# Kernel optimization log

Hardware: AMD Instinct MI355X
Metric: run time of the kernel (lower is better)

## Reference

```python
import jax, jax.numpy as jnp
import numpy as np

B, L, D, K, V = 256, 50, 128, 4, 50000
LENGTH = 5      # opt.length
BETA = 0.01     # opt.beta scaling on loss1
EPS = 1e-12     # F.normalize eps


def _l2norm(x, axis):
    n = jnp.sqrt(jnp.sum(x * x, axis=axis, keepdims=True))
    return x / jnp.maximum(n, EPS)


def setup_inputs() -> dict:
    key = jax.random.key(0)
    ks = jax.random.split(key, 11)
    s = 1.0 / np.sqrt(D)  # reset_parameters: uniform(-stdv, stdv)
    u = lambda k, shape: jax.random.uniform(k, shape, jnp.float32, -s, s)
    return {
        "hidden": jax.random.normal(ks[0], (B, L, D), jnp.float32),
        "mask": jnp.ones((B, L), jnp.int32),
        "pos_emb": u(ks[1], (L, D)),
        "w1": u(ks[2], (2 * D, D)),
        "w2": u(ks[3], (D, K)),
        "glu1_w": u(ks[4], (D, K * D)),
        "glu1_b": u(ks[5], (K * D,)),
        "att_w1": u(ks[6], (D, D)),
        "att_w2": u(ks[7], (D, D)),
        "att_v": u(ks[8], (D, K)),
        "emb": u(ks[9], (V, D)),
    }


def reference(hidden, mask, pos_emb, w1, w2, glu1_w, glu1_b, att_w1, att_w2, att_v, emb):
    m = mask.astype(jnp.float32)[..., None]                       # [B,L,1]
    hs = jnp.sum(hidden * m, axis=1) / jnp.sum(m, axis=1)         # [B,D] masked mean
    # nh = tanh(cat(pos, hidden) @ w1); then sigmoid(glu1)
    cat = jnp.concatenate([jnp.broadcast_to(pos_emb[None], hidden.shape), hidden], axis=-1)
    nh = jnp.tanh(cat @ w1)                                       # [B,L,D]
    nh = jax.nn.sigmoid(nh @ glu1_w + glu1_b)                     # [B,L,K*D]
    # torch.split(dim=2) + stack(dim=3) -> [B,L,D,K]
    nh = nh.reshape(B, L, K, D).transpose(0, 1, 3, 2)             # [B,L,D,K]
    beta = jnp.einsum('bldk,dk->blk', nh, w2)                     # [B,L,K]
    # attention gate alpha = sigmoid(att_v(tanh(W1 hs + W2 hidden)))
    att = jnp.tanh(hs[:, None, :] @ att_w1 + hidden @ att_w2)     # [B,L,D]
    alpha = jax.nn.sigmoid(att @ att_v)                           # [B,L,K]
    beta = beta * (0.5 + alpha) * m                               # mask over interests
    # per-interest L2 normalize along sequence (fused over K)
    nb = _l2norm(beta, axis=1)                                    # [B,L,K]
    # pairwise |cos| between interests: vectorized Gram instead of python loops
    G = jnp.einsum('bli,blj->bij', nb, nb)                        # [B,K,K]
    triu = jnp.triu(jnp.ones((K, K), jnp.float32), 1)
    sim = jnp.sum(jnp.abs(G) * triu, axis=(1, 2)) * (2.0 / (K * (K - 1)))  # [B]
    lens = jnp.sum(mask, axis=1).astype(jnp.float32) - LENGTH     # sumask[:,0] - length
    loss1 = jnp.sum(jax.nn.sigmoid(sim * lens))                   # scalar
    # per-interest pooled session reps, stacked on leading axis -> [K,B,D]
    select = jnp.einsum('blk,bld->kbd', beta, hidden)
    b_norm = _l2norm(emb[1:], axis=-1)                            # [V-1,D]
    scores = jnp.einsum('kbd,vd->kbv', select, b_norm)            # [K,B,V-1]
    max_scores = jnp.max(scores, axis=0)                          # [B,V-1]
    return (max_scores, loss1 * BETA, scores)
```

## Files before the change

kernel.cpp:

```cpp
#include <hip/hip_runtime.h>
#include <hip/hip_bf16.h>
#include <math.h>

constexpr int NB = 256;
constexpr int NL = 50;
constexpr int ND = 128;
constexpr int NK = 4;
constexpr int NVm1 = 49999;
constexpr int NPAD2 = 50176;
constexpr int ROWS = NB * NL;
constexpr int MROWS = NB * NK;
constexpr int GEMM_NT = 4;
constexpr int MR = 64;

constexpr int G_BN  = NPAD2 / 2;
constexpr int G_HS  = NB / 2;
constexpr int G_PP  = NL / 2;
constexpr int G_XB  = ROWS * ND / 2048;
constexpr int G_W1T = ND * ND / 256;
constexpr int G_AWT = ND * ND / 256;
constexpr int G_GLT = ND * 512 / 256;
constexpr int G_TOT = G_BN + G_HS + G_PP + G_XB + G_W1T + G_AWT + G_GLT;

typedef __bf16 bf16x8 __attribute__((ext_vector_type(8)));
typedef float f32x4 __attribute__((ext_vector_type(4)));

__device__ __forceinline__ float sigm_fast(float x) { return 1.0f / (1.0f + __expf(-x)); }
__device__ __forceinline__ float sigm_prec(float x) { return 1.0f / (1.0f + expf(-x)); }
__device__ __forceinline__ float fast_tanh(float x) {
    float xc = fminf(fmaxf(x, -15.f), 15.f);
    float e = __expf(2.f * xc);
    return (e - 1.f) / (e + 1.f);
}

__device__ __forceinline__ void gld_lds16(const void* g, void* l) {
    __builtin_amdgcn_global_load_lds(
        (const __attribute__((address_space(1))) void*)g,
        (__attribute__((address_space(3))) void*)l, 16, 0, 0);
}

__global__ __launch_bounds__(256) void k_prep(
    const float* __restrict__ hidden, const int* __restrict__ mask,
    const float* __restrict__ pos_emb, const float* __restrict__ w1,
    const float* __restrict__ att_w2, const float* __restrict__ glu1_w,
    const float* __restrict__ emb,
    float* __restrict__ hs, float* __restrict__ posPart,
    __hip_bfloat16* __restrict__ XbG, __hip_bfloat16* __restrict__ w1h_t,
    __hip_bfloat16* __restrict__ attw2_t, __hip_bfloat16* __restrict__ glu_t,
    __hip_bfloat16* __restrict__ bnv, float* __restrict__ loss_out) {
    __shared__ float sPP[2 * ND];
    __shared__ float red[4];
    int blk = blockIdx.x, tid = threadIdx.x;
    if (blk < G_BN) {
        int v = blk * 2 + (tid >> 7);
        int j = tid & 127;
        float x = 0.f;
        if (v < NVm1) x = emb[((size_t)v + 1) * ND + j];
        float ss = x * x;
        for (int off = 32; off >= 1; off >>= 1) ss += __shfl_xor(ss, off);
        if ((tid & 63) == 0) red[tid >> 6] = ss;
        __syncthreads();
        float tot = (tid < 128) ? (red[0] + red[1]) : (red[2] + red[3]);
        float rn = 1.f / fmaxf(sqrtf(tot), 1e-12f);
        bnv[(size_t)v * ND + j] = __float2bfloat16(x * rn);
    } else if (blk < G_BN + G_HS) {
        int b = (blk - G_BN) * 2 + (tid >> 7);
        int d = tid & 127;
        float acc = 0.f, msum = 0.f;
        for (int l = 0; l < NL; ++l) {
            float mv = (float)mask[b * NL + l];
            acc += hidden[((size_t)b * NL + l) * ND + d] * mv;
            msum += mv;
        }
        hs[b * ND + d] = acc / msum;
        if (blk == G_BN && tid == 0) loss_out[0] = 0.f;
    } else if (blk < G_BN + G_HS + G_PP) {
        int rel = blk - (G_BN + G_HS);
        int rl = tid >> 7, d = tid & 127;
        int r = rel * 2 + rl;
        sPP[rl * ND + d] = pos_emb[r * ND + d];
        __syncthreads();
        float acc = 0.f;
#pragma unroll 8
        for (int j = 0; j < ND; ++j) acc += sPP[rl * ND + j] * w1[j * ND + d];
        posPart[r * ND + d] = acc;
    } else if (blk < G_BN + G_HS + G_PP + G_XB) {
        int rel = blk - (G_BN + G_HS + G_PP);
        size_t base = (size_t)rel * 2048 + (size_t)tid * 8;
        float4 f0 = *(const float4*)&hidden[base];
        float4 f1 = *(const float4*)&hidden[base + 4];
        union { bf16x8 v; __hip_bfloat16 h[8]; } u;
        u.h[0] = __float2bfloat16(f0.x); u.h[1] = __float2bfloat16(f0.y);
        u.h[2] = __float2bfloat16(f0.z); u.h[3] = __float2bfloat16(f0.w);
        u.h[4] = __float2bfloat16(f1.x); u.h[5] = __float2bfloat16(f1.y);
        u.h[6] = __float2bfloat16(f1.z); u.h[7] = __float2bfloat16(f1.w);
        *(bf16x8*)&XbG[base] = u.v;
    } else if (blk < G_BN + G_HS + G_PP + G_XB + G_W1T) {
        int i = (blk - (G_BN + G_HS + G_PP + G_XB)) * 256 + tid;
        int d = i >> 7, j = i & 127;
        w1h_t[d * ND + j] = __float2bfloat16(w1[(ND + j) * ND + d]);
    } else if (blk < G_BN + G_HS + G_PP + G_XB + G_W1T + G_AWT) {
        int i = (blk - (G_BN + G_HS + G_PP + G_XB + G_W1T)) * 256 + tid;
        int d = i >> 7, j = i & 127;
        attw2_t[d * ND + j] = __float2bfloat16(att_w2[j * ND + d]);
    } else {
        int i = (blk - (G_BN + G_HS + G_PP + G_XB + G_W1T + G_AWT)) * 256 + tid;
        int c = i >> 7, j = i & 127;
        glu_t[c * ND + j] = __float2bfloat16(glu1_w[j * 512 + c]);
    }
}

__global__ __launch_bounds__(256) void k_mega(
    const __hip_bfloat16* __restrict__ XbG, const __hip_bfloat16* __restrict__ w1h_t,
    const __hip_bfloat16* __restrict__ attw2_t, const __hip_bfloat16* __restrict__ glu_t,
    const float* __restrict__ hs, const float* __restrict__ att_w1,
    const float* __restrict__ att_v, const float* __restrict__ posPart,
    const float* __restrict__ glu1_b, const float* __restrict__ w2,
    const int* __restrict__ mask, float* __restrict__ beta_out) {
    __shared__ __hip_bfloat16 XbS[MR * ND];
    __shared__ __hip_bfloat16 WS[ND * ND];
    __shared__ __attribute__((aligned(16))) __hip_bfloat16 NHS[MR * 136];
    __shared__ float alphaS[MR * NK];
    __shared__ float hsW1S[3 * ND];
    int row0 = blockIdx.x * MR;
    int tid = threadIdx.x;
    int wave = tid >> 6, lane = tid & 63, l16 = lane & 15, quad = lane >> 4;
    int b0 = row0 / NL;

#pragma unroll
    for (int it = 0; it < 4; ++it) {
        int id = it * 256 + tid;
        int row = id >> 4, c = id & 15, gc = c ^ (row & 7);
        gld_lds16((const char*)XbG + ((size_t)(row0 + row) * 16 + gc) * 16,
                  (char*)XbS + (size_t)(it * 256 + wave * 64) * 16);
    }
#pragma unroll
    for (int it = 0; it < 8; ++it) {
        int id = it * 256 + tid;
        int row = id >> 4, c = id & 15, gc = c ^ (row & 7);
        gld_lds16((const char*)attw2_t + ((size_t)row * 16 + gc) * 16,
                  (char*)WS + (size_t)(it * 256 + wave * 64) * 16);
    }
    for (int i = tid; i < 3 * ND; i += 256) {
        int bb = i >> 7, d = i & 127, b = b0 + bb;
        float acc = 0.f;
        if (b < NB) {
            for (int j = 0; j < ND; ++j) acc += hs[b * ND + j] * att_w1[j * ND + d];
        }
        hsW1S[i] = acc;
    }
    __syncthreads();

    const bf16x8* Xv = (const bf16x8*)XbS;
    const bf16x8* Wv = (const bf16x8*)WS;
    const bf16x8* Nv = (const bf16x8*)NHS;
    int arow = wave * 16 + l16;

    f32x4 acc8[8];
#pragma unroll
    for (int ni = 0; ni < 8; ++ni) acc8[ni] = (f32x4){0.f, 0.f, 0.f, 0.f};
#pragma unroll
    for (int kk = 0; kk < 4; ++kk) {
        int ko = kk * 4 + quad;
        bf16x8 af = Xv[arow * 16 + (ko ^ (arow & 7))];
#pragma unroll
        for (int ni = 0; ni < 8; ++ni) {
            int n = ni * 16 + l16;
            bf16x8 bf = Wv[n * 16 + (ko ^ (n & 7))];
            acc8[ni] = __builtin_amdgcn_mfma_f32_16x16x32_bf16(af, bf, acc8[ni], 0, 0, 0);
        }
    }
#pragma unroll
    for (int r = 0; r < 4; ++r) {
        int lrow = wave * 16 + quad * 4 + r;
        int grow = row0 + lrow;
        int bb = grow / NL - b0;
        float a0 = 0.f, a1 = 0.f, a2 = 0.f, a3 = 0.f;
#pragma unroll
        for (int ni = 0; ni < 8; ++ni) {
            int col = ni * 16 + l16;
            float atv = fast_tanh(hsW1S[bb * ND + col] + acc8[ni][r]);
            float4 av = *(const float4*)&att_v[col * 4];
            a0 += atv * av.x; a1 += atv * av.y; a2 += atv * av.z; a3 += atv * av.w;
        }
#pragma unroll
        for (int off = 1; off < 16; off <<= 1) {
            a0 += __shfl_xor(a0, off); a1 += __shfl_xor(a1, off);
            a2 += __shfl_xor(a2, off); a3 += __shfl_xor(a3, off);
        }
        if (l16 == 0) {
            alphaS[lrow * 4 + 0] = sigm_fast(a0);
            alphaS[lrow * 4 + 1] = sigm_fast(a1);
            alphaS[lrow * 4 + 2] = sigm_fast(a2);
            alphaS[lrow * 4 + 3] = sigm_fast(a3);
        }
    }
    __syncthreads();
#pragma unroll
    for (int it = 0; it < 8; ++it) {
        int id = it * 256 + tid;
        int row = id >> 4, c = id & 15, gc = c ^ (row & 7);
        gld_lds16((const char*)w1h_t + ((size_t)row * 16 + gc) * 16,
                  (char*)WS + (size_t)(it * 256 + wave * 64) * 16);
    }
    __syncthreads();
#pragma unroll
    for (int ni = 0; ni < 8; ++ni) acc8[ni] = (f32x4){0.f, 0.f, 0.f, 0.f};
#pragma unroll
    for (int kk = 0; kk < 4; ++kk) {
        int ko = kk * 4 + quad;
        bf16x8 af = Xv[arow * 16 + (ko ^ (arow & 7))];
#pragma unroll
        for (int ni = 0; ni < 8; ++ni) {
            int n = ni * 16 + l16;
            bf16x8 bf = Wv[n * 16 + (ko ^ (n & 7))];
            acc8[ni] = __builtin_amdgcn_mfma_f32_16x16x32_bf16(af, bf, acc8[ni], 0, 0, 0);
        }
    }
#pragma unroll
    for (int r = 0; r < 4; ++r) {
        int lrow = wave * 16 + quad * 4 + r;
        int grow = row0 + lrow;
        int l = grow % NL;
#pragma unroll
        for (int ni = 0; ni < 8; ++ni) {
            int col = ni * 16 + l16;
            float nhv = fast_tanh(posPart[l * ND + col] + acc8[ni][r]);
            NHS[lrow * 136 + col] = __float2bfloat16(nhv);
        }
    }
    __syncthreads();
    for (int ch = 0; ch < 4; ++ch) {
#pragma unroll
        for (int it = 0; it < 8; ++it) {
            int id = it * 256 + tid;
            int row = id >> 4, c = id & 15, gc = c ^ (row & 7);
            gld_lds16((const char*)glu_t + ((size_t)(ch * ND + row) * 16 + gc) * 16,
                      (char*)WS + (size_t)(it * 256 + wave * 64) * 16);
        }
        __syncthreads();
#pragma unroll
        for (int ni = 0; ni < 8; ++ni) acc8[ni] = (f32x4){0.f, 0.f, 0.f, 0.f};
#pragma unroll
        for (int kk = 0; kk < 4; ++kk) {
            int ko = kk * 4 + quad;
            bf16x8 af = Nv[arow * 17 + ko];
#pragma unroll
            for (int ni = 0; ni < 8; ++ni) {
                int n = ni * 16 + l16;
                bf16x8 bf = Wv[n * 16 + (ko ^ (n & 7))];
                acc8[ni] = __builtin_amdgcn_mfma_f32_16x16x32_bf16(af, bf, acc8[ni], 0, 0, 0);
            }
        }
#pragma unroll
        for (int r = 0; r < 4; ++r) {
            float s = 0.f;
#pragma unroll
            for (int ni = 0; ni < 8; ++ni) {
                int col = ni * 16 + l16;
                s += sigm_fast(acc8[ni][r] + glu1_b[ch * ND + col]) * w2[col * 4 + ch];
            }
#pragma unroll
            for (int off = 1; off < 16; off <<= 1) s += __shfl_xor(s, off);
            if (l16 == 0) {
                int lrow = wave * 16 + quad * 4 + r;
                int grow = row0 + lrow;
                float a = alphaS[lrow * 4 + ch];
                beta_out[(size_t)grow * 4 + ch] = s * (0.5f + a) * (float)mask[grow];
            }
        }
        __syncthreads();
    }
}

__global__ void k_loss(const float* __restrict__ beta, const int* __restrict__ mask,
                       float* __restrict__ loss_out) {
    int b = blockIdx.x;
    int t = threadIdx.x;
    float mv = (t < NL) ? (float)mask[b * NL + t] : 0.f;
    float msum = mv;
    for (int off = 32; off >= 1; off >>= 1) msum += __shfl_xor(msum, off);
    float lens = msum - 5.0f;
    float bk[NK] = {0.f, 0.f, 0.f, 0.f};
    if (t < NL) {
#pragma unroll
        for (int k = 0; k < NK; ++k) bk[k] = beta[((size_t)b * NL + t) * NK + k];
    }
    float nb[NK];
#pragma unroll
    for (int k = 0; k < NK; ++k) {
        float v = bk[k] * bk[k];
        for (int off = 32; off >= 1; off >>= 1) v += __shfl_xor(v, off);
        nb[k] = bk[k] / fmaxf(sqrtf(v), 1e-12f);
    }
    float sim = 0.f;
#pragma unroll
    for (int i = 0; i < NK; ++i) {
#pragma unroll
        for (int j = 0; j < NK; ++j) {
            if (j > i) {
                float p = nb[i] * nb[j];
                for (int off = 32; off >= 1; off >>= 1) p += __shfl_xor(p, off);
                sim += fabsf(p);
            }
        }
    }
    sim *= (2.0f / (NK * (NK - 1)));
    if (t == 0) atomicAdd(loss_out, sigm_prec(sim * lens) * 0.01f);
}

__global__ __launch_bounds__(256) void k_select(
    const float* __restrict__ beta, const float* __restrict__ hidden,
    __hip_bfloat16* __restrict__ selb) {
    int b = blockIdx.x * 2 + (threadIdx.x >> 7);
    int d = threadIdx.x & 127;
    float a0 = 0.f, a1 = 0.f, a2 = 0.f, a3 = 0.f;
    for (int l = 0; l < NL; ++l) {
        float h = hidden[((size_t)b * NL + l) * ND + d];
        const float* bp = &beta[((size_t)b * NL + l) * NK];
        a0 = fmaf(bp[0], h, a0);
        a1 = fmaf(bp[1], h, a1);
        a2 = fmaf(bp[2], h, a2);
        a3 = fmaf(bp[3], h, a3);
    }
    selb[((size_t)b * NK + 0) * ND + d] = __float2bfloat16(a0);
    selb[((size_t)b * NK + 1) * ND + d] = __float2bfloat16(a1);
    selb[((size_t)b * NK + 2) * ND + d] = __float2bfloat16(a2);
    selb[((size_t)b * NK + 3) * ND + d] = __float2bfloat16(a3);
}

__global__ __launch_bounds__(256) void k_gemm(
    const __hip_bfloat16* __restrict__ selb, const __hip_bfloat16* __restrict__ bn,
    float* __restrict__ scores, float* __restrict__ maxs) {
    __shared__ __hip_bfloat16 As[128 * 128];
    __shared__ __hip_bfloat16 Bs[128 * 128];
    int bm0 = blockIdx.y * 128;
    int nbase = blockIdx.x * (128 * GEMM_NT);
    int tid = threadIdx.x;
    int wave = tid >> 6, lane = tid & 63;
    int l16 = lane & 15, quad = lane >> 4;
    int m_loc = (wave >> 1) * 64;
    int n_loc = (wave & 1) * 64;

#pragma unroll
    for (int it = 0; it < 8; ++it) {
        int id = it * 256 + tid;
        int row = id >> 4, c = id & 15, gc = c ^ (row & 7);
        gld_lds16((const char*)selb + ((size_t)(bm0 + row) * 16 + gc) * 16,
                  (char*)As + (size_t)(it * 256 + wave * 64) * 16);
    }

    const bf16x8* Av = (const bf16x8*)As;
    const bf16x8* Bv = (const bf16x8*)Bs;

    for (int nt = 0; nt < GEMM_NT; ++nt) {
        int bn0 = nbase + nt * 128;
#pragma unroll
        for (int it = 0; it < 8; ++it) {
            int id = it * 256 + tid;
            int row = id >> 4, c = id & 15, gc = c ^ (row & 7);
            gld_lds16((const char*)bn + ((size_t)(bn0 + row) * 16 + gc) * 16,
                      (char*)Bs + (size_t)(it * 256 + wave * 64) * 16);
        }
        __syncthreads();

        f32x4 acc[4][4];
#pragma unroll
        for (int mi = 0; mi < 4; ++mi)
#pragma unroll
            for (int ni = 0; ni < 4; ++ni) acc[mi][ni] = (f32x4){0.f, 0.f, 0.f, 0.f};

#pragma unroll
        for (int kk = 0; kk < 4; ++kk) {
            int ko = kk * 4 + quad;
            bf16x8 afr[4], bfr[4];
#pragma unroll
            for (int mi = 0; mi < 4; ++mi) {
                int row = m_loc + mi * 16 + l16;
                afr[mi] = Av[row * 16 + (ko ^ (row & 7))];
            }
#pragma unroll
            for (int ni = 0; ni < 4; ++ni) {
                int row = n_loc + ni * 16 + l16;
                bfr[ni] = Bv[row * 16 + (ko ^ (row & 7))];
            }
#pragma unroll
            for (int mi = 0; mi < 4; ++mi)
#pragma unroll
                for (int ni = 0; ni < 4; ++ni)
                    acc[mi][ni] = __builtin_amdgcn_mfma_f32_16x16x32_bf16(
                        afr[mi], bfr[ni], acc[mi][ni], 0, 0, 0);
        }

#pragma unroll
        for (int mi = 0; mi < 4; ++mi) {
            int m_base = bm0 + m_loc + mi * 16;
            int bidx = (m_base >> 2) + quad;
#pragma unroll
            for (int ni = 0; ni < 4; ++ni) {
                int n = bn0 + n_loc + ni * 16 + l16;
                if (n < NVm1) {
                    float mx = acc[mi][ni][0];
#pragma unroll
                    for (int r = 0; r < 4; ++r) {
                        float val = acc[mi][ni][r];
                        scores[(size_t)r * NB * NVm1 + (size_t)bidx * NVm1 + n] = val;
                        mx = fmaxf(mx, val);
                    }
                    maxs[(size_t)bidx * NVm1 + n] = mx;
                }
            }
        }
        __syncthreads();
    }
}

extern "C" void kernel_launch(void* const* d_in, const int* in_sizes, int n_in,
                              void* d_out, int out_size, void* d_ws, size_t ws_size,
                              hipStream_t stream) {
    const float* hidden  = (const float*)d_in[0];
    const int*   mask    = (const int*)d_in[1];
    const float* pos_emb = (const float*)d_in[2];
    const float* w1      = (const float*)d_in[3];
    const float* w2      = (const float*)d_in[4];
    const float* glu1_w  = (const float*)d_in[5];
    const float* glu1_b  = (const float*)d_in[6];
    const float* att_w1  = (const float*)d_in[7];
    const float* att_w2  = (const float*)d_in[8];
    const float* att_v   = (const float*)d_in[9];
    const float* emb     = (const float*)d_in[10];

    float* out      = (float*)d_out;
    float* max_out  = out;
    float* loss_out = out + (size_t)NB * NVm1;
    float* scores   = out + (size_t)NB * NVm1 + 1;

    char* w = (char*)d_ws;
    auto alloc = [&](size_t bytes) {
        char* p = w;
        w += (bytes + 255) & ~(size_t)255;
        return p;
    };
    float* posPart = (float*)alloc((size_t)NL * ND * 4);
    float* hs      = (float*)alloc((size_t)NB * ND * 4);
    float* betav   = (float*)alloc((size_t)ROWS * NK * 4);
    __hip_bfloat16* XbG     = (__hip_bfloat16*)alloc((size_t)ROWS * ND * 2);
    __hip_bfloat16* w1h_t   = (__hip_bfloat16*)alloc((size_t)ND * ND * 2);
    __hip_bfloat16* attw2_t = (__hip_bfloat16*)alloc((size_t)ND * ND * 2);
    __hip_bfloat16* glu_t   = (__hip_bfloat16*)alloc((size_t)512 * ND * 2);
    __hip_bfloat16* selb    = (__hip_bfloat16*)alloc((size_t)MROWS * ND * 2);
    __hip_bfloat16* bnv     = (__hip_bfloat16*)alloc((size_t)NPAD2 * ND * 2);

    k_prep<<<G_TOT, 256, 0, stream>>>(hidden, mask, pos_emb, w1, att_w2, glu1_w, emb,
                                      hs, posPart, XbG, w1h_t, attw2_t, glu_t, bnv, loss_out);
    k_mega<<<ROWS / MR, 256, 0, stream>>>(XbG, w1h_t, attw2_t, glu_t, hs, att_w1,
                                          att_v, posPart, glu1_b, w2, mask, betav);
    k_loss<<<NB, 64, 0, stream>>>(betav, mask, loss_out);
    k_select<<<NB / 2, 256, 0, stream>>>(betav, hidden, selb);
    k_gemm<<<dim3(NPAD2 / (128 * GEMM_NT), MROWS / 128), 256, 0, stream>>>(selb, bnv, scores, max_out);
}
```

Baseline: 435.8 us.

## Double-buffer GEMM B tiles with nontemporal stores and vectorize embedding normalization

The scores GEMM now streams B in 64-column chunks through a double-buffered LDS tile. The next chunk's global-to-LDS load is issued before the current chunk's MFMAs, and full tiles wait with a partial vmcnt so the score stores stay in flight. Score and max outputs use nontemporal stores to cut cache pollution on the large output write. The embedding normalization in k_prep moves from a 2-rows-per-block LDS reduction to 8 rows per block using float4 loads and a 32-lane shuffle, and k_select reads beta as float4. The hand-tuned vmcnt value depends on the exact count of outstanding stores and loads, so any miscount could race.

```diff
diff --git a/kernel.cpp b/kernel.cpp
--- a/kernel.cpp
+++ b/kernel.cpp
@@ -10,10 +10,10 @@
 constexpr int NPAD2 = 50176;
 constexpr int ROWS = NB * NL;
 constexpr int MROWS = NB * NK;
-constexpr int GEMM_NT = 4;
+constexpr int GEMM_NSPAN = 512;
 constexpr int MR = 64;
 
-constexpr int G_BN  = NPAD2 / 2;
+constexpr int G_BN  = NPAD2 / 8;
 constexpr int G_HS  = NB / 2;
 constexpr int G_PP  = NL / 2;
 constexpr int G_XB  = ROWS * ND / 2048;
@@ -49,20 +49,22 @@
     __hip_bfloat16* __restrict__ attw2_t, __hip_bfloat16* __restrict__ glu_t,
     __hip_bfloat16* __restrict__ bnv, float* __restrict__ loss_out) {
     __shared__ float sPP[2 * ND];
-    __shared__ float red[4];
     int blk = blockIdx.x, tid = threadIdx.x;
     if (blk < G_BN) {
-        int v = blk * 2 + (tid >> 7);
-        int j = tid & 127;
-        float x = 0.f;
-        if (v < NVm1) x = emb[((size_t)v + 1) * ND + j];
-        float ss = x * x;
-        for (int off = 32; off >= 1; off >>= 1) ss += __shfl_xor(ss, off);
-        if ((tid & 63) == 0) red[tid >> 6] = ss;
-        __syncthreads();
-        float tot = (tid < 128) ? (red[0] + red[1]) : (red[2] + red[3]);
-        float rn = 1.f / fmaxf(sqrtf(tot), 1e-12f);
-        bnv[(size_t)v * ND + j] = __float2bfloat16(x * rn);
+        int v = blk * 8 + (tid >> 5);
+        int j = (tid & 31) << 2;
+        float4 x = make_float4(0.f, 0.f, 0.f, 0.f);
+        if (v < NVm1) x = *(const float4*)&emb[((size_t)v + 1) * ND + j];
+        float ss = x.x * x.x + x.y * x.y + x.z * x.z + x.w * x.w;
+#pragma unroll
+        for (int off = 16; off >= 1; off >>= 1) ss += __shfl_xor(ss, off);
+        float rn = 1.f / fmaxf(sqrtf(ss), 1e-12f);
+        union { ushort4 u4; __hip_bfloat16 h[4]; } o;
+        o.h[0] = __float2bfloat16(x.x * rn);
+        o.h[1] = __float2bfloat16(x.y * rn);
+        o.h[2] = __float2bfloat16(x.z * rn);
+        o.h[3] = __float2bfloat16(x.w * rn);
+        *(ushort4*)&bnv[(size_t)v * ND + j] = o.u4;
     } else if (blk < G_BN + G_HS) {
         int b = (blk - G_BN) * 2 + (tid >> 7);
         int d = tid & 127;
@@ -317,11 +319,11 @@
     float a0 = 0.f, a1 = 0.f, a2 = 0.f, a3 = 0.f;
     for (int l = 0; l < NL; ++l) {
         float h = hidden[((size_t)b * NL + l) * ND + d];
-        const float* bp = &beta[((size_t)b * NL + l) * NK];
-        a0 = fmaf(bp[0], h, a0);
-        a1 = fmaf(bp[1], h, a1);
-        a2 = fmaf(bp[2], h, a2);
-        a3 = fmaf(bp[3], h, a3);
+        float4 bv = *(const float4*)&beta[((size_t)b * NL + l) * NK];
+        a0 = fmaf(bv.x, h, a0);
+        a1 = fmaf(bv.y, h, a1);
+        a2 = fmaf(bv.z, h, a2);
+        a3 = fmaf(bv.w, h, a3);
     }
     selb[((size_t)b * NK + 0) * ND + d] = __float2bfloat16(a0);
     selb[((size_t)b * NK + 1) * ND + d] = __float2bfloat16(a1);
@@ -332,15 +334,16 @@
 __global__ __launch_bounds__(256) void k_gemm(
     const __hip_bfloat16* __restrict__ selb, const __hip_bfloat16* __restrict__ bn,
     float* __restrict__ scores, float* __restrict__ maxs) {
-    __shared__ __hip_bfloat16 As[128 * 128];
-    __shared__ __hip_bfloat16 Bs[128 * 128];
+    __shared__ __attribute__((aligned(16))) __hip_bfloat16 As[128 * 128];
+    __shared__ __attribute__((aligned(16))) __hip_bfloat16 Bs[2][64 * 128];
     int bm0 = blockIdx.y * 128;
-    int nbase = blockIdx.x * (128 * GEMM_NT);
+    int nbase = blockIdx.x * GEMM_NSPAN;
     int tid = threadIdx.x;
     int wave = tid >> 6, lane = tid & 63;
     int l16 = lane & 15, quad = lane >> 4;
-    int m_loc = (wave >> 1) * 64;
-    int n_loc = (wave & 1) * 64;
+    int m_loc = wave * 32;
+    bool full = (nbase + GEMM_NSPAN) <= NVm1;
+    const size_t SC_K = (size_t)NB * NVm1;
 
 #pragma unroll
     for (int it = 0; it < 8; ++it) {
@@ -349,69 +352,89 @@
         gld_lds16((const char*)selb + ((size_t)(bm0 + row) * 16 + gc) * 16,
                   (char*)As + (size_t)(it * 256 + wave * 64) * 16);
     }
+#pragma unroll
+    for (int it = 0; it < 4; ++it) {
+        int id = it * 256 + tid;
+        int row = id >> 4, c = id & 15, gc = c ^ (row & 7);
+        gld_lds16((const char*)bn + ((size_t)(nbase + row) * 16 + gc) * 16,
+                  (char*)Bs[0] + (size_t)(it * 256 + wave * 64) * 16);
+    }
+    __syncthreads();
 
     const bf16x8* Av = (const bf16x8*)As;
-    const bf16x8* Bv = (const bf16x8*)Bs;
-
-    for (int nt = 0; nt < GEMM_NT; ++nt) {
-        int bn0 = nbase + nt * 128;
-#pragma unroll
-        for (int it = 0; it < 8; ++it) {
-            int id = it * 256 + tid;
-            int row = id >> 4, c = id & 15, gc = c ^ (row & 7);
-            gld_lds16((const char*)bn + ((size_t)(bn0 + row) * 16 + gc) * 16,
-                      (char*)Bs + (size_t)(it * 256 + wave * 64) * 16);
-        }
-        __syncthreads();
-
-        f32x4 acc[4][4];
-#pragma unroll
-        for (int mi = 0; mi < 4; ++mi)
+
+#pragma unroll
+    for (int ch = 0; ch < 8; ++ch) {
+        if (ch < 7) {
+            int bn0 = nbase + (ch + 1) * 64;
+#pragma unroll
+            for (int it = 0; it < 4; ++it) {
+                int id = it * 256 + tid;
+                int row = id >> 4, c = id & 15, gc = c ^ (row & 7);
+                gld_lds16((const char*)bn + ((size_t)(bn0 + row) * 16 + gc) * 16,
+                          (char*)Bs[(ch + 1) & 1] + (size_t)(it * 256 + wave * 64) * 16);
+            }
+            __builtin_amdgcn_sched_barrier(0);
+        }
+        const bf16x8* Bv = (const bf16x8*)Bs[ch & 1];
+        f32x4 acc[2][4];
+#pragma unroll
+        for (int mi = 0; mi < 2; ++mi)
 #pragma unroll
             for (int ni = 0; ni < 4; ++ni) acc[mi][ni] = (f32x4){0.f, 0.f, 0.f, 0.f};
 
 #pragma unroll
         for (int kk = 0; kk < 4; ++kk) {
             int ko = kk * 4 + quad;
-            bf16x8 afr[4], bfr[4];
-#pragma unroll
-            for (int mi = 0; mi < 4; ++mi) {
+            bf16x8 afr[2], bfr[4];
+#pragma unroll
+            for (int mi = 0; mi < 2; ++mi) {
                 int row = m_loc + mi * 16 + l16;
                 afr[mi] = Av[row * 16 + (ko ^ (row & 7))];
             }
 #pragma unroll
             for (int ni = 0; ni < 4; ++ni) {
-                int row = n_loc + ni * 16 + l16;
+                int row = ni * 16 + l16;
                 bfr[ni] = Bv[row * 16 + (ko ^ (row & 7))];
             }
 #pragma unroll
-            for (int mi = 0; mi < 4; ++mi)
+            for (int mi = 0; mi < 2; ++mi)
 #pragma unroll
                 for (int ni = 0; ni < 4; ++ni)
                     acc[mi][ni] = __builtin_amdgcn_mfma_f32_16x16x32_bf16(
                         afr[mi], bfr[ni], acc[mi][ni], 0, 0, 0);
         }
 
-#pragma unroll
-        for (int mi = 0; mi < 4; ++mi) {
+        int ncol0 = nbase + ch * 64;
+#pragma unroll
+        for (int mi = 0; mi < 2; ++mi) {
             int m_base = bm0 + m_loc + mi * 16;
             int bidx = (m_base >> 2) + quad;
 #pragma unroll
             for (int ni = 0; ni < 4; ++ni) {
-                int n = bn0 + n_loc + ni * 16 + l16;
-                if (n < NVm1) {
+                int n = ncol0 + ni * 16 + l16;
+                if (full || n < NVm1) {
                     float mx = acc[mi][ni][0];
 #pragma unroll
                     for (int r = 0; r < 4; ++r) {
                         float val = acc[mi][ni][r];
-                        scores[(size_t)r * NB * NVm1 + (size_t)bidx * NVm1 + n] = val;
+                        __builtin_nontemporal_store(
+                            val, &scores[(size_t)r * SC_K + (size_t)bidx * NVm1 + n]);
                         mx = fmaxf(mx, val);
                     }
-                    maxs[(size_t)bidx * NVm1 + n] = mx;
+                    __builtin_nontemporal_store(mx, &maxs[(size_t)bidx * NVm1 + n]);
                 }
             }
         }
-        __syncthreads();
+
+        if (ch < 7) {
+            if (full) {
+                asm volatile("s_waitcnt vmcnt(40) lgkmcnt(0)" ::: "memory");
+                __builtin_amdgcn_s_barrier();
+            } else {
+                __syncthreads();
+            }
+        }
     }
 }
 
@@ -457,5 +480,5 @@
                                           att_v, posPart, glu1_b, w2, mask, betav);
     k_loss<<<NB, 64, 0, stream>>>(betav, mask, loss_out);
     k_select<<<NB / 2, 256, 0, stream>>>(betav, hidden, selb);
-    k_gemm<<<dim3(NPAD2 / (128 * GEMM_NT), MROWS / 128), 256, 0, stream>>>(selb, bnv, scores, max_out);
-}
+    k_gemm<<<dim3(NPAD2 / GEMM_NSPAN, MROWS / 128), 256, 0, stream>>>(selb, bnv, scores, max_out);
+}
```

Result: slower. 579.6 us (+33.0%).
